# Kernel optimization log

Measured on AMD Instinct MI355X. Metric: run time of the kernel, lower is better.

## Reference

```python
import jax, jax.numpy as jnp
import numpy as np

B, L, F = 256, 512, 64
NUM_IDS = 2000
LN_EPS = 1e-5


def setup_inputs() -> dict:
    key = jax.random.key(0)
    ks = jax.random.split(key, 16)
    s = 0.05
    return {
        # padded neighbor-id sequences; 0 is the padding id
        "src_ids": jax.random.randint(ks[0], (B, L), 0, NUM_IDS, dtype=jnp.int64)
        if jax.config.jax_enable_x64 else jax.random.randint(ks[0], (B, L), 0, NUM_IDS, dtype=jnp.int32),
        "dst_ids": jax.random.randint(ks[1], (B, L), 0, NUM_IDS, dtype=jnp.int64)
        if jax.config.jax_enable_x64 else jax.random.randint(ks[1], (B, L), 0, NUM_IDS, dtype=jnp.int32),
        # co-occurrence encode MLP: Linear(1->F), ReLU, Linear(F->F)
        "enc_w1": jax.random.normal(ks[2], (1, F), jnp.float32) * s,
        "enc_b1": jax.random.normal(ks[3], (F,), jnp.float32) * s,
        "enc_w2": jax.random.normal(ks[4], (F, F), jnp.float32) * s,
        "enc_b2": jax.random.normal(ks[5], (F,), jnp.float32) * s,
        # cross-attention projections (bias-free q/k/v as in source)
        "Wq": jax.random.normal(ks[6], (F, F), jnp.float32) * s,
        "Wk": jax.random.normal(ks[7], (F, F), jnp.float32) * s,
        "Wv": jax.random.normal(ks[8], (F, F), jnp.float32) * s,
        "Wo": jax.random.normal(ks[9], (F, F), jnp.float32) * s,
        "bo": jax.random.normal(ks[10], (F,), jnp.float32) * s,
        "ln_g": jnp.ones((F,), jnp.float32),
        "ln_b": jnp.zeros((F,), jnp.float32),
    }


def _counts_in(a, b):
    # for each element of a: how many times does it occur in b (same batch row)
    # equivalent to the np.unique count / mapping-dict lookup in the original
    return (a[:, :, None] == b[:, None, :]).sum(axis=-1).astype(jnp.float32)


def _appearances(a, b):
    # [B, L, 2]: counts of each id of `a` in (a, b); zero out padding (id==0)
    app = jnp.stack([_counts_in(a, a), _counts_in(a, b)], axis=-1)
    return jnp.where((a == 0)[..., None], 0.0, app)


def _encode(app, w1, b1, w2, b2):
    # Linear(1->F) -> ReLU -> Linear(F->F), then sum over the 2 count channels
    h = jax.nn.relu(app[..., None] * w1[0] + b1)  # [B, L, 2, F]
    h = jnp.einsum('blcf,fg->blcg', h, w2) + b2
    return h.sum(axis=2)  # [B, L, F]


def _linear_attn(q, k, v):
    dim = q.shape[-1]
    q = jax.nn.softmax(q, axis=-1) * (dim ** -0.5)
    k = jax.nn.softmax(k, axis=1)  # softmax over sequence dim (dim=-2)
    ctx = jnp.einsum('bld,ble->bde', k, v)
    return jnp.einsum('bld,bde->ble', q, ctx)


def _layer_norm(x, g, b):
    mu = x.mean(axis=-1, keepdims=True)
    var = ((x - mu) ** 2).mean(axis=-1, keepdims=True)
    return (x - mu) * jax.lax.rsqrt(var + LN_EPS) * g + b


def _cross_attn(x, ctx, Wq, Wk, Wv, Wo, bo, ln_g, ln_b):
    q, k, v = x @ Wq, ctx @ Wk, ctx @ Wv
    attn = _linear_attn(q, k, v)
    return _layer_norm(x + attn @ Wo + bo, ln_g, ln_b)


def reference(src_ids, dst_ids, enc_w1, enc_b1, enc_w2, enc_b2,
              Wq, Wk, Wv, Wo, bo, ln_g, ln_b):
    # neighbor co-occurrence counting + encoding
    src_app = _appearances(src_ids, dst_ids)  # [B, L, 2]
    dst_app = _appearances(dst_ids, src_ids)
    src_feat = _encode(src_app, enc_w1, enc_b1, enc_w2, enc_b2)  # [B, L, F]
    dst_feat = _encode(dst_app, enc_w1, enc_b1, enc_w2, enc_b2)
    # linear cross-attention fusion (shared weights, both directions)
    src_out = _cross_attn(src_feat, dst_feat, Wq, Wk, Wv, Wo, bo, ln_g, ln_b)
    dst_out = _cross_attn(dst_feat, src_feat, Wq, Wk, Wv, Wo, bo, ln_g, ln_b)
    return jnp.stack([src_out, dst_out])  # [2, B, L, F]
```

## Files before the change

### kernel.cpp

```cpp
#include <hip/hip_runtime.h>
#include <hip/hip_bf16.h>

#define BB 256
#define LL 512
#define FF 64
#define NIDS 2000

#define WS_TABLE 0
#define WS_PIDX  32832
#define WS_PKEY  (32832 + 262144)
#define WS_PMULT (32832 + 524288)
#define WS_NPAIR (32832 + 786432)

__global__ __launch_bounds__(64) void k_table(
    const float* __restrict__ w1, const float* __restrict__ b1,
    const float* __restrict__ w2, const float* __restrict__ b2,
    float* __restrict__ table) {
  int c = blockIdx.x, f = threadIdx.x;
  __shared__ float h[64];
  h[f] = fmaxf((float)c * w1[f] + b1[f], 0.f);
  __syncthreads();
  float acc = b2[f];
#pragma unroll
  for (int g = 0; g < 64; ++g) acc += h[g] * w2[g * 64 + f];
  table[c * 64 + f] = acc;
}

__global__ __launch_bounds__(256) void k_dedup(
    const int* __restrict__ src, const int* __restrict__ dst,
    int* __restrict__ pidx, int* __restrict__ pkey,
    int* __restrict__ pmult, int* __restrict__ npair) {
  int b = blockIdx.x, tid = threadIdx.x;
  __shared__ int hs[NIDS], hd[NIDS];
  __shared__ int hkey[1024], hmult[1024], hidx[1024];
  __shared__ int np;
  for (int i = tid; i < NIDS; i += 256) { hs[i] = 0; hd[i] = 0; }
  __syncthreads();
  const int* s = src + b * LL;
  const int* d = dst + b * LL;
  int sid0 = s[tid], sid1 = s[tid + 256];
  int did0 = d[tid], did1 = d[tid + 256];
  atomicAdd(&hs[sid0], 1); atomicAdd(&hs[sid1], 1);
  atomicAdd(&hd[did0], 1); atomicAdd(&hd[did1], 1);
  __syncthreads();
  for (int side = 0; side < 2; ++side) {
    for (int i = tid; i < 1024; i += 256) { hkey[i] = -1; hmult[i] = 0; }
    if (tid == 0) np = 0;
    __syncthreads();
    int slot[2];
    for (int r = 0; r < 2; ++r) {
      int id = (side == 0) ? (r ? sid1 : sid0) : (r ? did1 : did0);
      int ca = 0, cb = 0;
      if (id != 0) {
        if (side == 0) { ca = hs[id]; cb = hd[id]; }
        else           { ca = hd[id]; cb = hs[id]; }
      }
      int key = ca | (cb << 10);
      int h = (int)(((unsigned)key * 2654435761u) >> 22) & 1023;
      while (true) {
        int old = atomicCAS(&hkey[h], -1, key);
        if (old == -1 || old == key) break;
        h = (h + 1) & 1023;
      }
      atomicAdd(&hmult[h], 1);
      slot[r] = h;
    }
    __syncthreads();
    for (int i = tid; i < 1024; i += 256) {
      if (hkey[i] != -1) {
        int idx = atomicAdd(&np, 1);
        hidx[i] = idx;
        pkey [(side * BB + b) * LL + idx] = hkey[i];
        pmult[(side * BB + b) * LL + idx] = hmult[i];
      }
    }
    __syncthreads();
    pidx[(side * BB + b) * LL + tid]       = hidx[slot[0]];
    pidx[(side * BB + b) * LL + tid + 256] = hidx[slot[1]];
    if (tid == 0) npair[side * BB + b] = np;
    __syncthreads();
  }
}

__global__ __launch_bounds__(256, 2) void k_attn(
    const float* __restrict__ table,
    const int* __restrict__ pidx, const int* __restrict__ pkey,
    const int* __restrict__ pmult, const int* __restrict__ npair,
    const float* __restrict__ Wq, const float* __restrict__ Wk,
    const float* __restrict__ Wv, const float* __restrict__ Wo,
    const float* __restrict__ bo, const float* __restrict__ lng,
    const float* __restrict__ lnb, float* __restrict__ out) {
  int bd = blockIdx.x;
  int b = bd >> 1, dir = bd & 1;
  int tid = threadIdx.x, tx = tid & 63, ty = tid >> 6;

  __shared__ float featb[4][64];
  __shared__ float pbuf[4][64];
  __shared__ float vbuf[4][64];
  __shared__ float sred[4][64];
  __shared__ float M[64 * 65];
  __shared__ float G[64 * 65];
  __shared__ float wS[64 * 64];
  __shared__ int pidxl[512];
  __shared__ int xkeyb[512];
  __shared__ int ckeyb[512];
  __shared__ int cmultb[512];

  int xs = dir, cs = 1 - dir;
  for (int i = tid; i < 512; i += 256) {
    pidxl[i]  = pidx [(xs * BB + b) * LL + i];
    xkeyb[i]  = pkey [(xs * BB + b) * LL + i];
    ckeyb[i]  = pkey [(cs * BB + b) * LL + i];
    cmultb[i] = pmult[(cs * BB + b) * LL + i];
  }
  int Pc = npair[cs * BB + b];
  int Px = npair[xs * BB + b];

  float wcA[64], wcB[64];
#pragma unroll
  for (int f = 0; f < 64; ++f) { wcA[f] = Wk[f * 64 + tx]; wcB[f] = Wv[f * 64 + tx]; }
  float macc[16];
#pragma unroll
  for (int e = 0; e < 16; ++e) macc[e] = 0.f;
  float sacc = 0.f;
  __syncthreads();

  for (int j0 = 0; j0 < Pc; j0 += 4) {
    int j = j0 + ty;
    if (j < Pc) {
      int key = ckeyb[j];
      int ca = key & 1023, cb = key >> 10;
      featb[ty][tx] = table[ca * 64 + tx] + table[cb * 64 + tx];
      float kr = 0.f, vr = 0.f;
      const float4* fb4 = (const float4*)(&featb[ty][0]);
#pragma unroll
      for (int f4 = 0; f4 < 16; ++f4) {
        float4 fv = fb4[f4];
        kr += fv.x * wcA[4 * f4] + fv.y * wcA[4 * f4 + 1] + fv.z * wcA[4 * f4 + 2] + fv.w * wcA[4 * f4 + 3];
        vr += fv.x * wcB[4 * f4] + fv.y * wcB[4 * f4 + 1] + fv.z * wcB[4 * f4 + 2] + fv.w * wcB[4 * f4 + 3];
      }
      float p = __expf(kr) * (float)cmultb[j];
      sacc += p;
      pbuf[ty][tx] = p;
      vbuf[ty][tx] = vr;
    }
    __syncthreads();
    int jn = min(4, Pc - j0);
    int e0 = ty * 16;
    for (int jj = 0; jj < jn; ++jj) {
      float pg = pbuf[jj][tx];
      const float4* vb4 = (const float4*)(&vbuf[jj][e0]);
#pragma unroll
      for (int q = 0; q < 4; ++q) {
        float4 vv = vb4[q];
        macc[4 * q]     += pg * vv.x; macc[4 * q + 1] += pg * vv.y;
        macc[4 * q + 2] += pg * vv.z; macc[4 * q + 3] += pg * vv.w;
      }
    }
    __syncthreads();
  }
  sred[ty][tx] = sacc;
  __syncthreads();
  float sg = sred[0][tx] + sred[1][tx] + sred[2][tx] + sred[3][tx];
  float inv = 1.f / sg;
  int e0 = ty * 16;
#pragma unroll
  for (int e = 0; e < 16; ++e) M[tx * 65 + e0 + e] = macc[e] * inv;
  for (int i = tid; i < 4096; i += 256) wS[i] = Wo[i];
  __syncthreads();

#pragma unroll
  for (int e = 0; e < 16; ++e) macc[e] = 0.f;
  for (int e = 0; e < 64; ++e) {
    float m = M[tx * 65 + e];
    const float4* wo4 = (const float4*)(&wS[e * 64 + e0]);
#pragma unroll
    for (int q = 0; q < 4; ++q) {
      float4 w4 = wo4[q];
      macc[4 * q]     += m * w4.x; macc[4 * q + 1] += m * w4.y;
      macc[4 * q + 2] += m * w4.z; macc[4 * q + 3] += m * w4.w;
    }
  }
#pragma unroll
  for (int e = 0; e < 16; ++e) G[tx * 65 + e0 + e] = macc[e];
#pragma unroll
  for (int f = 0; f < 64; ++f) wcA[f] = Wq[f * 64 + tx];
  float bov = bo[tx], lg = lng[tx], lb = lnb[tx];
  __syncthreads();

  for (int i0 = 0; i0 < Px; i0 += 64) {
    int cN = min(64, Px - i0);
    for (int jj = ty; jj < cN; jj += 4) {
      int key = xkeyb[i0 + jj];
      int ca = key & 1023, cb = key >> 10;
      float fv = table[ca * 64 + tx] + table[cb * 64 + tx];
      featb[ty][tx] = fv;
      float qr = 0.f;
      const float4* fb4 = (const float4*)(&featb[ty][0]);
#pragma unroll
      for (int f4 = 0; f4 < 16; ++f4) {
        float4 f4v = fb4[f4];
        qr += f4v.x * wcA[4 * f4] + f4v.y * wcA[4 * f4 + 1] + f4v.z * wcA[4 * f4 + 2] + f4v.w * wcA[4 * f4 + 3];
      }
      float p = __expf(qr);
      float sum = p;
#pragma unroll
      for (int off = 32; off >= 1; off >>= 1) sum += __shfl_xor(sum, off, 64);
      float qh = p / sum * 0.125f;
      pbuf[ty][tx] = qh;
      float at = 0.f;
#pragma unroll
      for (int dd = 0; dd < 64; ++dd) at += pbuf[ty][dd] * G[dd * 65 + tx];
      float r = fv + at + bov;
      float mu = r;
#pragma unroll
      for (int off = 32; off >= 1; off >>= 1) mu += __shfl_xor(mu, off, 64);
      mu *= (1.f / 64.f);
      float dv = r - mu;
      float var = dv * dv;
#pragma unroll
      for (int off = 32; off >= 1; off >>= 1) var += __shfl_xor(var, off, 64);
      var *= (1.f / 64.f);
      wS[jj * 64 + tx] = dv * rsqrtf(var + 1e-5f) * lg + lb;
    }
    __syncthreads();
    const float4* w4 = (const float4*)wS;
    float4* out4 = (float4*)(out + (size_t)(dir * BB + b) * LL * 64);
    for (int idx = tid; idx < 512 * 16; idx += 256) {
      int l = idx >> 4, q = idx & 15;
      int pid = pidxl[l];
      if (pid >= i0 && pid < i0 + cN) out4[l * 16 + q] = w4[(pid - i0) * 16 + q];
    }
    __syncthreads();
  }
}

extern "C" void kernel_launch(void* const* d_in, const int* in_sizes, int n_in,
                              void* d_out, int out_size, void* d_ws, size_t ws_size,
                              hipStream_t stream) {
  const int* src  = (const int*)d_in[0];
  const int* dst  = (const int*)d_in[1];
  const float* w1 = (const float*)d_in[2];
  const float* b1 = (const float*)d_in[3];
  const float* w2 = (const float*)d_in[4];
  const float* b2 = (const float*)d_in[5];
  const float* Wq = (const float*)d_in[6];
  const float* Wk = (const float*)d_in[7];
  const float* Wv = (const float*)d_in[8];
  const float* Wo = (const float*)d_in[9];
  const float* bo = (const float*)d_in[10];
  const float* lng = (const float*)d_in[11];
  const float* lnb = (const float*)d_in[12];
  float* out = (float*)d_out;
  float* wsf = (float*)d_ws;
  int* wsi = (int*)d_ws;

  float* table = wsf + WS_TABLE;
  int* pidx  = wsi + WS_PIDX;
  int* pkey  = wsi + WS_PKEY;
  int* pmult = wsi + WS_PMULT;
  int* npair = wsi + WS_NPAIR;

  k_table<<<dim3(513), dim3(64), 0, stream>>>(w1, b1, w2, b2, table);
  k_dedup<<<dim3(256), dim3(256), 0, stream>>>(src, dst, pidx, pkey, pmult, npair);
  k_attn<<<dim3(512), dim3(256), 0, stream>>>(table, pidx, pkey, pmult, npair,
                                              Wq, Wk, Wv, Wo, bo, lng, lnb, out);
}
```

Baseline: 123.8 us.

## Fuse table build into dedup kernel and cut attention registers and LDS

Merges the encode-table kernel into the dedup kernel, so one launch is removed and each block computes two or three table rows. In the attention kernel, K and V projections are split into separate passes that reuse one weight register array. The per-row staging buffers are merged into one shared pool, and G is kept in registers per column. Together these aim for 3 blocks per CU instead of 2. Output writes become nontemporal stores, at the cost of more syncs and extra LDS traffic from chunking 32 context rows.

Measured after the change: 128.9 us. 1.04x slower.

```diff
diff --git a/kernel.cpp b/kernel.cpp
--- a/kernel.cpp
+++ b/kernel.cpp
@@ -3,8 +3,9 @@
 
 #define BB 256
 #define LL 512
-#define FF 64
 #define NIDS 2000
+
+typedef float nfloat4 __attribute__((ext_vector_type(4)));
 
 #define WS_TABLE 0
 #define WS_PIDX  32832
@@ -12,28 +13,28 @@
 #define WS_PMULT (32832 + 524288)
 #define WS_NPAIR (32832 + 786432)
 
-__global__ __launch_bounds__(64) void k_table(
+__global__ __launch_bounds__(256) void k_prep(
+    const int* __restrict__ src, const int* __restrict__ dst,
     const float* __restrict__ w1, const float* __restrict__ b1,
     const float* __restrict__ w2, const float* __restrict__ b2,
-    float* __restrict__ table) {
-  int c = blockIdx.x, f = threadIdx.x;
-  __shared__ float h[64];
-  h[f] = fmaxf((float)c * w1[f] + b1[f], 0.f);
-  __syncthreads();
-  float acc = b2[f];
-#pragma unroll
-  for (int g = 0; g < 64; ++g) acc += h[g] * w2[g * 64 + f];
-  table[c * 64 + f] = acc;
-}
-
-__global__ __launch_bounds__(256) void k_dedup(
-    const int* __restrict__ src, const int* __restrict__ dst,
+    float* __restrict__ table,
     int* __restrict__ pidx, int* __restrict__ pkey,
     int* __restrict__ pmult, int* __restrict__ npair) {
-  int b = blockIdx.x, tid = threadIdx.x;
+  int b = blockIdx.x, tid = threadIdx.x, tx = tid & 63, ty = tid >> 6;
   __shared__ int hs[NIDS], hd[NIDS];
   __shared__ int hkey[1024], hmult[1024], hidx[1024];
+  __shared__ float hb[4][64];
   __shared__ int np;
+
+  if (ty < 2 || (b == 255 && ty == 2)) {
+    int c = 2 * b + ty;
+    hb[ty][tx] = fmaxf((float)c * w1[tx] + b1[tx], 0.f);
+    float acc = b2[tx];
+#pragma unroll
+    for (int f = 0; f < 64; ++f) acc += hb[ty][f] * w2[f * 64 + tx];
+    table[c * 64 + tx] = acc;
+  }
+
   for (int i = tid; i < NIDS; i += 256) { hs[i] = 0; hd[i] = 0; }
   __syncthreads();
   const int* s = src + b * LL;
@@ -43,6 +44,7 @@
   atomicAdd(&hs[sid0], 1); atomicAdd(&hs[sid1], 1);
   atomicAdd(&hd[did0], 1); atomicAdd(&hd[did1], 1);
   __syncthreads();
+
   for (int side = 0; side < 2; ++side) {
     for (int i = tid; i < 1024; i += 256) { hkey[i] = -1; hmult[i] = 0; }
     if (tid == 0) np = 0;
@@ -82,7 +84,7 @@
   }
 }
 
-__global__ __launch_bounds__(256, 2) void k_attn(
+__global__ __launch_bounds__(256, 3) void k_attn(
     const float* __restrict__ table,
     const int* __restrict__ pidx, const int* __restrict__ pkey,
     const int* __restrict__ pmult, const int* __restrict__ npair,
@@ -94,13 +96,11 @@
   int b = bd >> 1, dir = bd & 1;
   int tid = threadIdx.x, tx = tid & 63, ty = tid >> 6;
 
+  __shared__ float pool[6144];
+  __shared__ float M[64 * 66];
   __shared__ float featb[4][64];
-  __shared__ float pbuf[4][64];
-  __shared__ float vbuf[4][64];
+  __shared__ float qbuf[4][64];
   __shared__ float sred[4][64];
-  __shared__ float M[64 * 65];
-  __shared__ float G[64 * 65];
-  __shared__ float wS[64 * 64];
   __shared__ int pidxl[512];
   __shared__ int xkeyb[512];
   __shared__ int ckeyb[512];
@@ -116,40 +116,49 @@
   int Pc = npair[cs * BB + b];
   int Px = npair[xs * BB + b];
 
-  float wcA[64], wcB[64];
-#pragma unroll
-  for (int f = 0; f < 64; ++f) { wcA[f] = Wk[f * 64 + tx]; wcB[f] = Wv[f * 64 + tx]; }
+  float wa[64];
   float macc[16];
 #pragma unroll
   for (int e = 0; e < 16; ++e) macc[e] = 0.f;
   float sacc = 0.f;
-  __syncthreads();
-
-  for (int j0 = 0; j0 < Pc; j0 += 4) {
-    int j = j0 + ty;
-    if (j < Pc) {
-      int key = ckeyb[j];
+  int e0 = ty * 16;
+  __syncthreads();
+
+  for (int j0 = 0; j0 < Pc; j0 += 32) {
+    int cN = min(32, Pc - j0);
+#pragma unroll
+    for (int f = 0; f < 64; ++f) wa[f] = Wk[f * 64 + tx];
+    for (int j = ty; j < cN; j += 4) {
+      int key = ckeyb[j0 + j];
       int ca = key & 1023, cb = key >> 10;
-      featb[ty][tx] = table[ca * 64 + tx] + table[cb * 64 + tx];
-      float kr = 0.f, vr = 0.f;
-      const float4* fb4 = (const float4*)(&featb[ty][0]);
-#pragma unroll
-      for (int f4 = 0; f4 < 16; ++f4) {
-        float4 fv = fb4[f4];
-        kr += fv.x * wcA[4 * f4] + fv.y * wcA[4 * f4 + 1] + fv.z * wcA[4 * f4 + 2] + fv.w * wcA[4 * f4 + 3];
-        vr += fv.x * wcB[4 * f4] + fv.y * wcB[4 * f4 + 1] + fv.z * wcB[4 * f4 + 2] + fv.w * wcB[4 * f4 + 3];
-      }
-      float p = __expf(kr) * (float)cmultb[j];
+      pool[j * 64 + tx] = table[ca * 64 + tx] + table[cb * 64 + tx];
+      float kr = 0.f;
+      const float4* fb4 = (const float4*)&pool[j * 64];
+#pragma unroll
+      for (int q = 0; q < 16; ++q) {
+        float4 fv = fb4[q];
+        kr += fv.x * wa[4 * q] + fv.y * wa[4 * q + 1] + fv.z * wa[4 * q + 2] + fv.w * wa[4 * q + 3];
+      }
+      float p = __expf(kr) * (float)cmultb[j0 + j];
       sacc += p;
-      pbuf[ty][tx] = p;
-      vbuf[ty][tx] = vr;
-    }
-    __syncthreads();
-    int jn = min(4, Pc - j0);
-    int e0 = ty * 16;
-    for (int jj = 0; jj < jn; ++jj) {
-      float pg = pbuf[jj][tx];
-      const float4* vb4 = (const float4*)(&vbuf[jj][e0]);
+      pool[2048 + j * 64 + tx] = p;
+    }
+#pragma unroll
+    for (int f = 0; f < 64; ++f) wa[f] = Wv[f * 64 + tx];
+    for (int j = ty; j < cN; j += 4) {
+      float vr = 0.f;
+      const float4* fb4 = (const float4*)&pool[j * 64];
+#pragma unroll
+      for (int q = 0; q < 16; ++q) {
+        float4 fv = fb4[q];
+        vr += fv.x * wa[4 * q] + fv.y * wa[4 * q + 1] + fv.z * wa[4 * q + 2] + fv.w * wa[4 * q + 3];
+      }
+      pool[4096 + j * 64 + tx] = vr;
+    }
+    __syncthreads();
+    for (int jj = 0; jj < cN; ++jj) {
+      float pg = pool[2048 + jj * 64 + tx];
+      const float4* vb4 = (const float4*)&pool[4096 + jj * 64 + e0];
 #pragma unroll
       for (int q = 0; q < 4; ++q) {
         float4 vv = vb4[q];
@@ -161,19 +170,17 @@
   }
   sred[ty][tx] = sacc;
   __syncthreads();
-  float sg = sred[0][tx] + sred[1][tx] + sred[2][tx] + sred[3][tx];
-  float inv = 1.f / sg;
-  int e0 = ty * 16;
-#pragma unroll
-  for (int e = 0; e < 16; ++e) M[tx * 65 + e0 + e] = macc[e] * inv;
-  for (int i = tid; i < 4096; i += 256) wS[i] = Wo[i];
+  float inv = 1.f / (sred[0][tx] + sred[1][tx] + sred[2][tx] + sred[3][tx]);
+#pragma unroll
+  for (int e = 0; e < 16; ++e) M[tx * 66 + e0 + e] = macc[e] * inv;
+  for (int i = tid; i < 4096; i += 256) pool[i] = Wo[i];
   __syncthreads();
 
 #pragma unroll
   for (int e = 0; e < 16; ++e) macc[e] = 0.f;
-  for (int e = 0; e < 64; ++e) {
-    float m = M[tx * 65 + e];
-    const float4* wo4 = (const float4*)(&wS[e * 64 + e0]);
+  for (int f = 0; f < 64; ++f) {
+    float m = M[tx * 66 + f];
+    const float4* wo4 = (const float4*)&pool[f * 64 + e0];
 #pragma unroll
     for (int q = 0; q < 4; ++q) {
       float4 w4 = wo4[q];
@@ -181,12 +188,16 @@
       macc[4 * q + 2] += m * w4.z; macc[4 * q + 3] += m * w4.w;
     }
   }
-#pragma unroll
-  for (int e = 0; e < 16; ++e) G[tx * 65 + e0 + e] = macc[e];
-#pragma unroll
-  for (int f = 0; f < 64; ++f) wcA[f] = Wq[f * 64 + tx];
+  __syncthreads();
+#pragma unroll
+  for (int e = 0; e < 16; ++e) M[tx * 66 + e0 + e] = macc[e];
+  __syncthreads();
+  float gcol[64];
+#pragma unroll
+  for (int dd = 0; dd < 64; ++dd) gcol[dd] = M[dd * 66 + tx];
+#pragma unroll
+  for (int f = 0; f < 64; ++f) wa[f] = Wq[f * 64 + tx];
   float bov = bo[tx], lg = lng[tx], lb = lnb[tx];
-  __syncthreads();
 
   for (int i0 = 0; i0 < Px; i0 += 64) {
     int cN = min(64, Px - i0);
@@ -196,21 +207,25 @@
       float fv = table[ca * 64 + tx] + table[cb * 64 + tx];
       featb[ty][tx] = fv;
       float qr = 0.f;
-      const float4* fb4 = (const float4*)(&featb[ty][0]);
-#pragma unroll
-      for (int f4 = 0; f4 < 16; ++f4) {
-        float4 f4v = fb4[f4];
-        qr += f4v.x * wcA[4 * f4] + f4v.y * wcA[4 * f4 + 1] + f4v.z * wcA[4 * f4 + 2] + f4v.w * wcA[4 * f4 + 3];
+      const float4* fb4 = (const float4*)&featb[ty][0];
+#pragma unroll
+      for (int q = 0; q < 16; ++q) {
+        float4 f4v = fb4[q];
+        qr += f4v.x * wa[4 * q] + f4v.y * wa[4 * q + 1] + f4v.z * wa[4 * q + 2] + f4v.w * wa[4 * q + 3];
       }
       float p = __expf(qr);
       float sum = p;
 #pragma unroll
       for (int off = 32; off >= 1; off >>= 1) sum += __shfl_xor(sum, off, 64);
       float qh = p / sum * 0.125f;
-      pbuf[ty][tx] = qh;
+      qbuf[ty][tx] = qh;
       float at = 0.f;
-#pragma unroll
-      for (int dd = 0; dd < 64; ++dd) at += pbuf[ty][dd] * G[dd * 65 + tx];
+      const float4* qb4 = (const float4*)&qbuf[ty][0];
+#pragma unroll
+      for (int q = 0; q < 16; ++q) {
+        float4 qv = qb4[q];
+        at += qv.x * gcol[4 * q] + qv.y * gcol[4 * q + 1] + qv.z * gcol[4 * q + 2] + qv.w * gcol[4 * q + 3];
+      }
       float r = fv + at + bov;
       float mu = r;
 #pragma unroll
@@ -221,15 +236,16 @@
 #pragma unroll
       for (int off = 32; off >= 1; off >>= 1) var += __shfl_xor(var, off, 64);
       var *= (1.f / 64.f);
-      wS[jj * 64 + tx] = dv * rsqrtf(var + 1e-5f) * lg + lb;
-    }
-    __syncthreads();
-    const float4* w4 = (const float4*)wS;
-    float4* out4 = (float4*)(out + (size_t)(dir * BB + b) * LL * 64);
+      pool[jj * 64 + tx] = dv * rsqrtf(var + 1e-5f) * lg + lb;
+    }
+    __syncthreads();
+    const nfloat4* w4 = (const nfloat4*)pool;
+    nfloat4* out4 = (nfloat4*)(out + (size_t)(dir * BB + b) * (LL * 64));
     for (int idx = tid; idx < 512 * 16; idx += 256) {
       int l = idx >> 4, q = idx & 15;
       int pid = pidxl[l];
-      if (pid >= i0 && pid < i0 + cN) out4[l * 16 + q] = w4[(pid - i0) * 16 + q];
+      if (pid >= i0 && pid < i0 + cN)
+        __builtin_nontemporal_store(w4[(pid - i0) * 16 + q], &out4[l * 16 + q]);
     }
     __syncthreads();
   }
@@ -261,8 +277,8 @@
   int* pmult = wsi + WS_PMULT;
   int* npair = wsi + WS_NPAIR;
 
-  k_table<<<dim3(513), dim3(64), 0, stream>>>(w1, b1, w2, b2, table);
-  k_dedup<<<dim3(256), dim3(256), 0, stream>>>(src, dst, pidx, pkey, pmult, npair);
+  k_prep<<<dim3(256), dim3(256), 0, stream>>>(src, dst, w1, b1, w2, b2,
+                                              table, pidx, pkey, pmult, npair);
   k_attn<<<dim3(512), dim3(256), 0, stream>>>(table, pidx, pkey, pmult, npair,
                                               Wq, Wk, Wv, Wo, bo, lng, lnb, out);
 }
```
